# Performance work log

Hardware: AMD Instinct MI355X
Metric: run time of the kernel (lower is better)

Reference implementation:

```python
import jax, jax.numpy as jnp
import numpy as np

B, T, D, H, K, V = 2, 2048, 2048, 16, 128, 128


def _l2norm(x, eps=1e-12):
    # F.normalize(p=2, dim=-1)
    n = jnp.sqrt(jnp.sum(x * x, axis=-1, keepdims=True))
    return x / jnp.maximum(n, eps)


def setup_inputs() -> dict:
    key = jax.random.key(0)
    ks = jax.random.split(key, 7)
    s = D ** -0.5
    return {
        "x": jax.random.normal(ks[0], (B, T, D), jnp.float32),
        "Wq": jax.random.normal(ks[1], (H * K, D), jnp.float32) * s,
        "Wk": jax.random.normal(ks[2], (H * K, D), jnp.float32) * s,
        "Wv": jax.random.normal(ks[3], (H * V, D), jnp.float32) * s,
        "Wa": jax.random.normal(ks[4], (H, D), jnp.float32) * s,
        "ba": jnp.zeros((H,), jnp.float32),
        "Wb": jax.random.normal(ks[5], (H, D), jnp.float32) * s,
        "bb": jnp.zeros((H,), jnp.float32),
    }


def _forward(x, Wq, Wk, Wv, Wa, ba, Wb, bb):
    Bq, Tq, _ = x.shape
    # projections (nn.Linear: y = x @ W.T)
    q = _l2norm(jnp.einsum('btd,od->bto', x, Wq).reshape(Bq, Tq, H, K))
    k = _l2norm(jnp.einsum('btd,od->bto', x, Wk).reshape(Bq, Tq, H, K))
    v = jnp.einsum('btd,od->bto', x, Wv).reshape(Bq, Tq, H, V)
    alpha = jax.nn.sigmoid(jnp.einsum('btd,hd->bth', x, Wa) + ba)          # [B,T,H] decay in (0,1)
    beta = jax.nn.softplus(jnp.einsum('btd,hd->bth', x, Wb) + bb) * K ** (-0.5)

    # gated delta rule recurrence over time (vectorized over B,H):
    #   S_t = a_t * S_{t-1} (I - b_t k_t k_t^T) + b_t v_t k_t^T ;  o_t = S_t q_t
    def step(S, inp):
        q_t, k_t, v_t, a_t, b_t = inp  # [B,H,K],[B,H,K],[B,H,V],[B,H],[B,H]
        Sd = S * a_t[..., None, None]                              # decay  [B,H,V,K]
        pred = jnp.einsum('bhvk,bhk->bhv', Sd, k_t)                # S k
        u = b_t[..., None] * (v_t - pred)                          # delta update [B,H,V]
        S_new = Sd + u[..., None] * k_t[:, :, None, :]             # rank-1 write
        o_t = jnp.einsum('bhvk,bhk->bhv', S_new, q_t)
        return S_new, o_t

    S0 = jnp.zeros((Bq, H, V, K), x.dtype)
    xs = (q.transpose(1, 0, 2, 3), k.transpose(1, 0, 2, 3),
          v.transpose(1, 0, 2, 3), alpha.transpose(1, 0, 2), beta.transpose(1, 0, 2))
    _, o = jax.lax.scan(step, S0, xs)
    return o.transpose(1, 0, 2, 3)  # [B,T,H,V]


def reference(x, Wq, Wk, Wv, Wa, ba, Wb, bb):
    return _forward(x, Wq, Wk, Wv, Wa, ba, Wb, bb)
```

## Files before the change

kernel.cpp:

```cpp
#include <hip/hip_runtime.h>
#include <math.h>

#define BB 2
#define TT 2048
#define DD 2048
#define HH 16
#define KK 128

typedef _Float16 h4 __attribute__((ext_vector_type(4)));
typedef _Float16 v8h __attribute__((ext_vector_type(8)));
typedef float v4f __attribute__((ext_vector_type(4)));
typedef unsigned int u2v __attribute__((ext_vector_type(2)));

__global__ __launch_bounds__(256) void gemm_nt3(const float* __restrict__ A,
                                                const float* __restrict__ W0,
                                                const float* __restrict__ W1,
                                                const float* __restrict__ W2,
                                                float* __restrict__ Cbase,
                                                int M, int N, int Kd) {
  __shared__ float As[8][128];
  __shared__ float Bs[8][128];
  const int z = blockIdx.z;
  const float* W = (z == 0) ? W0 : (z == 1) ? W1 : W2;
  float* C = Cbase + (size_t)z * M * N;
  const int tid = threadIdx.x;
  const int bm = blockIdx.y * 128;
  const int bn = blockIdx.x * 128;
  const int lrow = tid >> 1;
  const int lcol = (tid & 1) * 4;
  const int rm = (tid >> 4) * 8;
  const int rn = (tid & 15) * 8;
  const float* Ap = A + (size_t)(bm + lrow) * Kd + lcol;
  const float* Wp = W + (size_t)(bn + lrow) * Kd + lcol;
  float acc[8][8];
#pragma unroll
  for (int i = 0; i < 8; i++)
#pragma unroll
    for (int j = 0; j < 8; j++) acc[i][j] = 0.f;
  float4 av = *(const float4*)Ap;
  float4 wv = *(const float4*)Wp;
  for (int d0 = 0; d0 < Kd; d0 += 8) {
    __syncthreads();
    As[lcol + 0][lrow] = av.x; As[lcol + 1][lrow] = av.y;
    As[lcol + 2][lrow] = av.z; As[lcol + 3][lrow] = av.w;
    Bs[lcol + 0][lrow] = wv.x; Bs[lcol + 1][lrow] = wv.y;
    Bs[lcol + 2][lrow] = wv.z; Bs[lcol + 3][lrow] = wv.w;
    __syncthreads();
    if (d0 + 8 < Kd) {
      av = *(const float4*)(Ap + d0 + 8);
      wv = *(const float4*)(Wp + d0 + 8);
    }
#pragma unroll
    for (int kk = 0; kk < 8; kk++) {
      const float4 a0 = *(const float4*)&As[kk][rm];
      const float4 a1 = *(const float4*)&As[kk][rm + 4];
      const float4 b0 = *(const float4*)&Bs[kk][rn];
      const float4 b1 = *(const float4*)&Bs[kk][rn + 4];
      const float ar[8] = {a0.x, a0.y, a0.z, a0.w, a1.x, a1.y, a1.z, a1.w};
      const float br[8] = {b0.x, b0.y, b0.z, b0.w, b1.x, b1.y, b1.z, b1.w};
#pragma unroll
      for (int i = 0; i < 8; i++)
#pragma unroll
        for (int j = 0; j < 8; j++) acc[i][j] = fmaf(ar[i], br[j], acc[i][j]);
    }
  }
#pragma unroll
  for (int i = 0; i < 8; i++) {
    float* cp = C + (size_t)(bm + rm + i) * N + bn + rn;
    float4 c0 = {acc[i][0], acc[i][1], acc[i][2], acc[i][3]};
    float4 c1 = {acc[i][4], acc[i][5], acc[i][6], acc[i][7]};
    *(float4*)cp = c0;
    *(float4*)(cp + 4) = c1;
  }
}

__global__ __launch_bounds__(256) void convert_f16(
    const float* __restrict__ x, const float* __restrict__ Wq,
    const float* __restrict__ Wk, const float* __restrict__ Wv,
    _Float16* __restrict__ xh, _Float16* __restrict__ xl,
    _Float16* __restrict__ Wf) {
  const size_t N4X = (size_t)BB * TT * DD / 4;
  const size_t N4W = (size_t)(HH * KK) * DD / 4;
  const size_t i = (size_t)blockIdx.x * 256 + threadIdx.x;
  if (i < N4X) {
    const float4 v = ((const float4*)x)[i];
    h4 hi, lo;
    hi.x = (_Float16)v.x; hi.y = (_Float16)v.y;
    hi.z = (_Float16)v.z; hi.w = (_Float16)v.w;
    lo.x = (_Float16)(v.x - (float)hi.x);
    lo.y = (_Float16)(v.y - (float)hi.y);
    lo.z = (_Float16)(v.z - (float)hi.z);
    lo.w = (_Float16)(v.w - (float)hi.w);
    ((h4*)xh)[i] = hi;
    ((h4*)xl)[i] = lo;
  } else {
    const size_t j = i - N4X;
    const float* Ws = (j < N4W) ? Wq : (j < 2 * N4W) ? Wk : Wv;
    const size_t jj = (j < N4W) ? j : (j < 2 * N4W) ? (j - N4W) : (j - 2 * N4W);
    const float4 v = ((const float4*)Ws)[jj];
    h4 hi;
    hi.x = (_Float16)v.x; hi.y = (_Float16)v.y;
    hi.z = (_Float16)v.z; hi.w = (_Float16)v.w;
    ((h4*)Wf)[j] = hi;
  }
}

#define GLDS(gp, lp)                                              \
  __builtin_amdgcn_global_load_lds(                               \
      (const __attribute__((address_space(1))) void*)(gp),        \
      (__attribute__((address_space(3))) void*)(lp), 16, 0, 0)

__global__ __launch_bounds__(256) void gemm_mfma(
    const _Float16* __restrict__ xh, const _Float16* __restrict__ xl,
    const _Float16* __restrict__ Wf, float* __restrict__ Cbase) {
  __shared__ float4 lraw[1536];
  _Float16* Ah = (_Float16*)lraw;
  _Float16* Al = Ah + 4096;
  _Float16* Bs = Al + 4096;

  const int z = blockIdx.z;
  const _Float16* W = Wf + (size_t)z * DD * (HH * KK);
  float* C = Cbase + (size_t)z * (BB * TT) * (HH * KK);

  const int tid = threadIdx.x;
  const int w = tid >> 6;
  const int lane = tid & 63;
  const int bm = blockIdx.y * 128;
  const int bn = blockIdx.x * 128;
  const int wm = (w & 1) * 64;
  const int wn = (w >> 1) * 64;
  const int m16 = lane & 15;
  const int quad = lane >> 4;

  const _Float16* gAh = xh + (size_t)(bm + (tid >> 2)) * DD + (tid & 3) * 8;
  const _Float16* gAl = xl + (size_t)(bm + (tid >> 2)) * DD + (tid & 3) * 8;
  const _Float16* gB = W + (size_t)(bn + (tid >> 2)) * DD + (tid & 3) * 8;
  const int lb = w * 512;

  v4f acc[4][4];
#pragma unroll
  for (int i = 0; i < 4; i++)
#pragma unroll
    for (int j = 0; j < 4; j++) acc[i][j] = (v4f){0.f, 0.f, 0.f, 0.f};

  for (int d0 = 0; d0 < DD; d0 += 32) {
    GLDS(gAh + d0, Ah + lb);
    GLDS(gAh + d0 + 64 * DD, Ah + 2048 + lb);
    GLDS(gAl + d0, Al + lb);
    GLDS(gAl + d0 + 64 * DD, Al + 2048 + lb);
    GLDS(gB + d0, Bs + lb);
    GLDS(gB + d0 + 64 * DD, Bs + 2048 + lb);
    __syncthreads();
    v8h ah[4], al[4], bw[4];
#pragma unroll
    for (int i = 0; i < 4; i++) {
      ah[i] = *(const v8h*)&Ah[(wm + i * 16 + m16) * 32 + quad * 8];
      al[i] = *(const v8h*)&Al[(wm + i * 16 + m16) * 32 + quad * 8];
      bw[i] = *(const v8h*)&Bs[(wn + i * 16 + m16) * 32 + quad * 8];
    }
#pragma unroll
    for (int mi = 0; mi < 4; mi++)
#pragma unroll
      for (int ni = 0; ni < 4; ni++) {
        acc[mi][ni] = __builtin_amdgcn_mfma_f32_16x16x32_f16(ah[mi], bw[ni],
                                                             acc[mi][ni], 0, 0, 0);
        acc[mi][ni] = __builtin_amdgcn_mfma_f32_16x16x32_f16(al[mi], bw[ni],
                                                             acc[mi][ni], 0, 0, 0);
      }
    __syncthreads();
  }
#pragma unroll
  for (int mi = 0; mi < 4; mi++) {
#pragma unroll
    for (int r = 0; r < 4; r++) {
      float* cp =
          C + (size_t)(bm + wm + mi * 16 + quad * 4 + r) * (HH * KK) + bn + wn + m16;
#pragma unroll
      for (int ni = 0; ni < 4; ni++) cp[ni * 16] = acc[mi][ni][r];
    }
  }
}

__global__ __launch_bounds__(64) void ab_proj(const float* __restrict__ x,
                                              const float* __restrict__ Wa,
                                              const float* __restrict__ ba,
                                              const float* __restrict__ Wb,
                                              const float* __restrict__ bb,
                                              float* __restrict__ abq) {
  const int row = blockIdx.x;
  const int g = blockIdx.y;
  const int h0 = (g & 1) * 8;
  const bool isA = (g < 2);
  const float* W = isA ? Wa : Wb;
  const int lane = threadIdx.x;
  const float* xr = x + (size_t)row * DD;
  float acc[8];
#pragma unroll
  for (int j = 0; j < 8; j++) acc[j] = 0.f;
  for (int d = lane; d < DD; d += 64) {
    const float xv = xr[d];
#pragma unroll
    for (int j = 0; j < 8; j++)
      acc[j] = fmaf(xv, W[(size_t)(h0 + j) * DD + d], acc[j]);
  }
#pragma unroll
  for (int j = 0; j < 8; j++) {
#pragma unroll
    for (int off = 32; off > 0; off >>= 1) acc[j] += __shfl_xor(acc[j], off, 64);
  }
  if (lane == 0) {
    if (isA) {
#pragma unroll
      for (int j = 0; j < 8; j++) {
        const float z = acc[j] + ba[h0 + j];
        abq[((size_t)row * HH + h0 + j) * 4 + 0] = 1.0f / (1.0f + expf(-z));
      }
    } else {
#pragma unroll
      for (int j = 0; j < 8; j++) {
        const float z = acc[j] + bb[h0 + j];
        const float sp = (z > 20.f) ? z : log1pf(expf(z));
        abq[((size_t)row * HH + h0 + j) * 4 + 1] = sp * 0.08838834764831845f;
      }
    }
  }
}

__global__ __launch_bounds__(256) void norm_qk(float* __restrict__ q,
                                               float* __restrict__ k,
                                               float* __restrict__ abq) {
  const int vec = blockIdx.x * 4 + (threadIdx.x >> 6);
  const int l = threadIdx.x & 63;
  float* qp = q + (size_t)vec * 128;
  float* kp = k + (size_t)vec * 128;
  float q0 = qp[l], q1 = qp[l + 64];
  float k0 = kp[l], k1 = kp[l + 64];
  float sq = q0 * q0 + q1 * q1;
  float sk = k0 * k0 + k1 * k1;
#pragma unroll
  for (int off = 32; off > 0; off >>= 1) {
    sq += __shfl_xor(sq, off, 64);
    sk += __shfl_xor(sk, off, 64);
  }
  const float iq = 1.0f / fmaxf(sqrtf(sq), 1e-12f);
  const float ik = 1.0f / fmaxf(sqrtf(sk), 1e-12f);
  q0 *= iq; q1 *= iq; k0 *= ik; k1 *= ik;
  qp[l] = q0; qp[l + 64] = q1;
  kp[l] = k0; kp[l + 64] = k1;
  float pq = q0 * k0 + q1 * k1;
#pragma unroll
  for (int off = 32; off > 0; off >>= 1) pq += __shfl_xor(pq, off, 64);
  if (l == 0) abq[(size_t)vec * 4 + 2] = pq;
}

#define DPP_ADD(x, ctrl)                                                     \
  ((x) + __int_as_float(__builtin_amdgcn_update_dpp(                         \
             0, __float_as_int(x), (ctrl), 0xF, 0xF, true)))

__device__ __forceinline__ float xadd32(float x) {
  const u2v r = __builtin_amdgcn_permlane32_swap(__float_as_uint(x),
                                                 __float_as_uint(x), false,
                                                 false);
  return __uint_as_float(r.x) + __uint_as_float(r.y);
}

#define SCAN_STEP(kc, qc, vc, ac, store_ptr)                                   \
  {                                                                            \
    float dk = fmaf(S0, kc.x, fmaf(S1, kc.y, fmaf(S2, kc.z, S3 * kc.w)));      \
    float dq = fmaf(S0, qc.x, fmaf(S1, qc.y, fmaf(S2, qc.z, S3 * qc.w)));      \
    dk = DPP_ADD(dk, 0xB1);  dq = DPP_ADD(dq, 0xB1);             \
    dk = DPP_ADD(dk, 0x4E);  dq = DPP_ADD(dq, 0x4E);             \
    dk = DPP_ADD(dk, 0x141); dq = DPP_ADD(dq, 0x141);            \
    dk = DPP_ADD(dk, 0x140); dq = DPP_ADD(dq, 0x140);            \
    dk = xadd32(dk);         dq = xadd32(dq);                    \
    const float u = ac.y * fmaf(-ac.x, dk, vc);                                \
    const float oo = fmaf(ac.x, dq, u * ac.z);                                 \
    S0 = fmaf(ac.x, S0, u * kc.x);                                             \
    S1 = fmaf(ac.x, S1, u * kc.y);                                             \
    S2 = fmaf(ac.x, S2, u * kc.z);                                             \
    S3 = fmaf(ac.x, S3, u * kc.w);                                             \
    if (ks == 0) *(store_ptr) = oo;                                            \
  }

#define PD 8

__global__ __launch_bounds__(256, 2) void scan_kernel(
    const float* __restrict__ q, const float* __restrict__ k,
    const float* __restrict__ v, const float* __restrict__ abq,
    float* __restrict__ o) {
  const int bid = blockIdx.x;
  const int bh = bid & 31;
  const int s = bid >> 5;
  const int h = bh & 15;
  const int b = bh >> 4;
  const int tid = threadIdx.x;
  const int w = tid >> 6;
  const int lane = tid & 63;
  const int rg = (lane >> 4) & 1;
  const int ks = (lane & 15) | ((lane >> 5) << 4);
  const int vrow = s * 8 + w * 2 + rg;

  const size_t base = (size_t)b * TT * 2048 + (size_t)h * KK;
  const float* kb = k + base + ks * 4;
  const float* qb = q + base + ks * 4;
  const float* vb = v + base + vrow;
  const float* ab = abq + ((size_t)b * TT * HH + h) * 4;
  float* ob = o + base + vrow;

  float S0 = 0.f, S1 = 0.f, S2 = 0.f, S3 = 0.f;

  float4 kf[PD], qf[PD], af[PD];
  float vf[PD];
#pragma unroll
  for (int d = 0; d < PD; d++) {
    kf[d] = *(const float4*)(kb + d * 2048);
    qf[d] = *(const float4*)(qb + d * 2048);
    vf[d] = vb[d * 2048];
    af[d] = *(const float4*)(ab + d * 64);
  }

  int off = 0;
  int aoff = 0;
  for (int t0 = 0; t0 < TT - PD; t0 += PD) {
#pragma unroll
    for (int j = 0; j < PD; j++) {
      SCAN_STEP(kf[j], qf[j], vf[j], af[j], ob + off + j * 2048);
      kf[j] = *(const float4*)(kb + off + (j + PD) * 2048);
      qf[j] = *(const float4*)(qb + off + (j + PD) * 2048);
      vf[j] = vb[off + (j + PD) * 2048];
      af[j] = *(const float4*)(ab + aoff + (j + PD) * 64);
      __builtin_amdgcn_sched_barrier(0);
    }
    off += PD * 2048;
    aoff += PD * 64;
  }
#pragma unroll
  for (int j = 0; j < PD; j++) {
    SCAN_STEP(kf[j], qf[j], vf[j], af[j], ob + off + j * 2048);
  }
}

extern "C" void kernel_launch(void* const* d_in, const int* in_sizes, int n_in,
                              void* d_out, int out_size, void* d_ws,
                              size_t ws_size, hipStream_t stream) {
  const float* x = (const float*)d_in[0];
  const float* Wq = (const float*)d_in[1];
  const float* Wk = (const float*)d_in[2];
  const float* Wv = (const float*)d_in[3];
  const float* Wa = (const float*)d_in[4];
  const float* ba = (const float*)d_in[5];
  const float* Wb = (const float*)d_in[6];
  const float* bb = (const float*)d_in[7];
  float* out = (float*)d_out;
  float* ws = (float*)d_ws;

  const size_t PROJ = (size_t)BB * TT * HH * KK;
  const size_t NABQ = (size_t)BB * TT * HH * 4;
  float* qw = ws;
  float* kw = ws + PROJ;
  float* vw = ws + 2 * PROJ;
  float* abq = ws + 3 * PROJ;
  _Float16* xh = (_Float16*)(abq + NABQ);
  _Float16* xl = xh + (size_t)BB * TT * DD;
  _Float16* Wf = xl + (size_t)BB * TT * DD;
  const size_t NEED = (3 * PROJ + NABQ) * 4 +
                      ((size_t)BB * TT * DD * 2 + 3 * (size_t)(HH * KK) * DD) * 2;

  const int M = BB * TT;
  const int N = HH * KK;
  if (ws_size >= NEED) {
    const int cgrid = (int)(((size_t)BB * TT * DD / 4 + 3 * (size_t)N * DD / 4) / 256);
    convert_f16<<<cgrid, 256, 0, stream>>>(x, Wq, Wk, Wv, xh, xl, Wf);
    gemm_mfma<<<dim3(N / 128, M / 128, 3), 256, 0, stream>>>(xh, xl, Wf, qw);
  } else {
    gemm_nt3<<<dim3(N / 128, M / 128, 3), 256, 0, stream>>>(x, Wq, Wk, Wv, qw,
                                                            M, N, DD);
  }
  ab_proj<<<dim3(M, 4), 64, 0, stream>>>(x, Wa, ba, Wb, bb, abq);
  norm_qk<<<(BB * TT * HH) / 4, 256, 0, stream>>>(qw, kw, abq);
  scan_kernel<<<BB * HH * 16, 256, 0, stream>>>(qw, kw, vw, abq, out);
}
```

Before: 774.6 us.

## Drop fp16 lo-part of x in GEMM, pack scan state math, batch output stores

The projection GEMM no longer splits x into fp16 hi and lo parts. It uses one fp16 operand, which halves the MFMA count, the LDS traffic and the conversion writes, at the cost of accuracy in q/k/v. The scan kernel now holds its state in packed float2 vectors and uses elementwise FMA so the compiler can emit packed FP32 instructions. Outputs are buffered across the 8 unrolled steps and written by 8 lanes at once instead of one store per step.

```diff
diff --git a/kernel.cpp b/kernel.cpp
--- a/kernel.cpp
+++ b/kernel.cpp
@@ -10,6 +10,7 @@
 typedef _Float16 h4 __attribute__((ext_vector_type(4)));
 typedef _Float16 v8h __attribute__((ext_vector_type(8)));
 typedef float v4f __attribute__((ext_vector_type(4)));
+typedef float f2 __attribute__((ext_vector_type(2)));
 typedef unsigned int u2v __attribute__((ext_vector_type(2)));
 
 __global__ __launch_bounds__(256) void gemm_nt3(const float* __restrict__ A,
@@ -77,22 +78,16 @@
 __global__ __launch_bounds__(256) void convert_f16(
     const float* __restrict__ x, const float* __restrict__ Wq,
     const float* __restrict__ Wk, const float* __restrict__ Wv,
-    _Float16* __restrict__ xh, _Float16* __restrict__ xl,
-    _Float16* __restrict__ Wf) {
+    _Float16* __restrict__ xh, _Float16* __restrict__ Wf) {
   const size_t N4X = (size_t)BB * TT * DD / 4;
   const size_t N4W = (size_t)(HH * KK) * DD / 4;
   const size_t i = (size_t)blockIdx.x * 256 + threadIdx.x;
   if (i < N4X) {
     const float4 v = ((const float4*)x)[i];
-    h4 hi, lo;
+    h4 hi;
     hi.x = (_Float16)v.x; hi.y = (_Float16)v.y;
     hi.z = (_Float16)v.z; hi.w = (_Float16)v.w;
-    lo.x = (_Float16)(v.x - (float)hi.x);
-    lo.y = (_Float16)(v.y - (float)hi.y);
-    lo.z = (_Float16)(v.z - (float)hi.z);
-    lo.w = (_Float16)(v.w - (float)hi.w);
     ((h4*)xh)[i] = hi;
-    ((h4*)xl)[i] = lo;
   } else {
     const size_t j = i - N4X;
     const float* Ws = (j < N4W) ? Wq : (j < 2 * N4W) ? Wk : Wv;
@@ -111,12 +106,11 @@
       (__attribute__((address_space(3))) void*)(lp), 16, 0, 0)
 
 __global__ __launch_bounds__(256) void gemm_mfma(
-    const _Float16* __restrict__ xh, const _Float16* __restrict__ xl,
-    const _Float16* __restrict__ Wf, float* __restrict__ Cbase) {
-  __shared__ float4 lraw[1536];
+    const _Float16* __restrict__ xh, const _Float16* __restrict__ Wf,
+    float* __restrict__ Cbase) {
+  __shared__ float4 lraw[1024];
   _Float16* Ah = (_Float16*)lraw;
-  _Float16* Al = Ah + 4096;
-  _Float16* Bs = Al + 4096;
+  _Float16* Bs = Ah + 4096;
 
   const int z = blockIdx.z;
   const _Float16* W = Wf + (size_t)z * DD * (HH * KK);
@@ -132,8 +126,7 @@
   const int m16 = lane & 15;
   const int quad = lane >> 4;
 
-  const _Float16* gAh = xh + (size_t)(bm + (tid >> 2)) * DD + (tid & 3) * 8;
-  const _Float16* gAl = xl + (size_t)(bm + (tid >> 2)) * DD + (tid & 3) * 8;
+  const _Float16* gA = xh + (size_t)(bm + (tid >> 2)) * DD + (tid & 3) * 8;
   const _Float16* gB = W + (size_t)(bn + (tid >> 2)) * DD + (tid & 3) * 8;
   const int lb = w * 512;
 
@@ -144,29 +137,23 @@
     for (int j = 0; j < 4; j++) acc[i][j] = (v4f){0.f, 0.f, 0.f, 0.f};
 
   for (int d0 = 0; d0 < DD; d0 += 32) {
-    GLDS(gAh + d0, Ah + lb);
-    GLDS(gAh + d0 + 64 * DD, Ah + 2048 + lb);
-    GLDS(gAl + d0, Al + lb);
-    GLDS(gAl + d0 + 64 * DD, Al + 2048 + lb);
+    GLDS(gA + d0, Ah + lb);
+    GLDS(gA + d0 + 64 * DD, Ah + 2048 + lb);
     GLDS(gB + d0, Bs + lb);
     GLDS(gB + d0 + 64 * DD, Bs + 2048 + lb);
     __syncthreads();
-    v8h ah[4], al[4], bw[4];
+    v8h ah[4], bw[4];
 #pragma unroll
     for (int i = 0; i < 4; i++) {
       ah[i] = *(const v8h*)&Ah[(wm + i * 16 + m16) * 32 + quad * 8];
-      al[i] = *(const v8h*)&Al[(wm + i * 16 + m16) * 32 + quad * 8];
       bw[i] = *(const v8h*)&Bs[(wn + i * 16 + m16) * 32 + quad * 8];
     }
 #pragma unroll
     for (int mi = 0; mi < 4; mi++)
 #pragma unroll
-      for (int ni = 0; ni < 4; ni++) {
+      for (int ni = 0; ni < 4; ni++)
         acc[mi][ni] = __builtin_amdgcn_mfma_f32_16x16x32_f16(ah[mi], bw[ni],
                                                              acc[mi][ni], 0, 0, 0);
-        acc[mi][ni] = __builtin_amdgcn_mfma_f32_16x16x32_f16(al[mi], bw[ni],
-                                                             acc[mi][ni], 0, 0, 0);
-      }
     __syncthreads();
   }
 #pragma unroll
@@ -264,10 +251,16 @@
   return __uint_as_float(r.x) + __uint_as_float(r.y);
 }
 
-#define SCAN_STEP(kc, qc, vc, ac, store_ptr)                                   \
+#define SCAN_STEP(kc, qc, vc, ac, jj)                                          \
   {                                                                            \
-    float dk = fmaf(S0, kc.x, fmaf(S1, kc.y, fmaf(S2, kc.z, S3 * kc.w)));      \
-    float dq = fmaf(S0, qc.x, fmaf(S1, qc.y, fmaf(S2, qc.z, S3 * qc.w)));      \
+    const f2 ka = {kc.x, kc.y};                                                \
+    const f2 kb2 = {kc.z, kc.w};                                               \
+    const f2 qa = {qc.x, qc.y};                                                \
+    const f2 qb2 = {qc.z, qc.w};                                               \
+    const f2 pdk = __builtin_elementwise_fma(Sb, kb2, Sa * ka);                \
+    const f2 pdq = __builtin_elementwise_fma(Sb, qb2, Sa * qa);                \
+    float dk = pdk.x + pdk.y;                                                  \
+    float dq = pdq.x + pdq.y;                                                  \
     dk = DPP_ADD(dk, 0xB1);  dq = DPP_ADD(dq, 0xB1);             \
     dk = DPP_ADD(dk, 0x4E);  dq = DPP_ADD(dq, 0x4E);             \
     dk = DPP_ADD(dk, 0x141); dq = DPP_ADD(dq, 0x141);            \
@@ -275,11 +268,11 @@
     dk = xadd32(dk);         dq = xadd32(dq);                    \
     const float u = ac.y * fmaf(-ac.x, dk, vc);                                \
     const float oo = fmaf(ac.x, dq, u * ac.z);                                 \
-    S0 = fmaf(ac.x, S0, u * kc.x);                                             \
-    S1 = fmaf(ac.x, S1, u * kc.y);                                             \
-    S2 = fmaf(ac.x, S2, u * kc.z);                                             \
-    S3 = fmaf(ac.x, S3, u * kc.w);                                             \
-    if (ks == 0) *(store_ptr) = oo;                                            \
+    const f2 a2 = {ac.x, ac.x};                                                \
+    const f2 u2 = {u, u};                                                      \
+    Sa = __builtin_elementwise_fma(a2, Sa, u2 * ka);                           \
+    Sb = __builtin_elementwise_fma(a2, Sb, u2 * kb2);                          \
+    obuf = (ks == (jj)) ? oo : obuf;                                           \
   }
 
 #define PD 8
@@ -301,22 +294,24 @@
   const int vrow = s * 8 + w * 2 + rg;
 
   const size_t base = (size_t)b * TT * 2048 + (size_t)h * KK;
-  const float* kb = k + base + ks * 4;
-  const float* qb = q + base + ks * 4;
-  const float* vb = v + base + vrow;
-  const float* ab = abq + ((size_t)b * TT * HH + h) * 4;
-  float* ob = o + base + vrow;
-
-  float S0 = 0.f, S1 = 0.f, S2 = 0.f, S3 = 0.f;
+  const float* kU = k + base;
+  const float* qU = q + base;
+  const float* vU = v + base;
+  const float* aU = abq + ((size_t)b * TT * HH + h) * 4;
+  float* oU = o + base;
+  const int vks = ks * 4;
+
+  f2 Sa = {0.f, 0.f}, Sb = {0.f, 0.f};
+  float obuf = 0.f;
 
   float4 kf[PD], qf[PD], af[PD];
   float vf[PD];
 #pragma unroll
   for (int d = 0; d < PD; d++) {
-    kf[d] = *(const float4*)(kb + d * 2048);
-    qf[d] = *(const float4*)(qb + d * 2048);
-    vf[d] = vb[d * 2048];
-    af[d] = *(const float4*)(ab + d * 64);
+    kf[d] = *(const float4*)(kU + vks + d * 2048);
+    qf[d] = *(const float4*)(qU + vks + d * 2048);
+    vf[d] = vU[vrow + d * 2048];
+    af[d] = *(const float4*)(aU + d * 64);
   }
 
   int off = 0;
@@ -324,20 +319,22 @@
   for (int t0 = 0; t0 < TT - PD; t0 += PD) {
 #pragma unroll
     for (int j = 0; j < PD; j++) {
-      SCAN_STEP(kf[j], qf[j], vf[j], af[j], ob + off + j * 2048);
-      kf[j] = *(const float4*)(kb + off + (j + PD) * 2048);
-      qf[j] = *(const float4*)(qb + off + (j + PD) * 2048);
-      vf[j] = vb[off + (j + PD) * 2048];
-      af[j] = *(const float4*)(ab + aoff + (j + PD) * 64);
+      SCAN_STEP(kf[j], qf[j], vf[j], af[j], j);
+      kf[j] = *(const float4*)(kU + vks + off + (j + PD) * 2048);
+      qf[j] = *(const float4*)(qU + vks + off + (j + PD) * 2048);
+      vf[j] = vU[vrow + off + (j + PD) * 2048];
+      af[j] = *(const float4*)(aU + aoff + (j + PD) * 64);
       __builtin_amdgcn_sched_barrier(0);
     }
+    if (ks < 8) oU[vrow + off + ks * 2048] = obuf;
     off += PD * 2048;
     aoff += PD * 64;
   }
 #pragma unroll
   for (int j = 0; j < PD; j++) {
-    SCAN_STEP(kf[j], qf[j], vf[j], af[j], ob + off + j * 2048);
-  }
+    SCAN_STEP(kf[j], qf[j], vf[j], af[j], j);
+  }
+  if (ks < 8) oU[vrow + off + ks * 2048] = obuf;
 }
 
 extern "C" void kernel_launch(void* const* d_in, const int* in_sizes, int n_in,
@@ -361,17 +358,16 @@
   float* vw = ws + 2 * PROJ;
   float* abq = ws + 3 * PROJ;
   _Float16* xh = (_Float16*)(abq + NABQ);
-  _Float16* xl = xh + (size_t)BB * TT * DD;
-  _Float16* Wf = xl + (size_t)BB * TT * DD;
+  _Float16* Wf = xh + (size_t)BB * TT * DD;
   const size_t NEED = (3 * PROJ + NABQ) * 4 +
-                      ((size_t)BB * TT * DD * 2 + 3 * (size_t)(HH * KK) * DD) * 2;
+                      ((size_t)BB * TT * DD + 3 * (size_t)(HH * KK) * DD) * 2;
 
   const int M = BB * TT;
   const int N = HH * KK;
   if (ws_size >= NEED) {
     const int cgrid = (int)(((size_t)BB * TT * DD / 4 + 3 * (size_t)N * DD / 4) / 256);
-    convert_f16<<<cgrid, 256, 0, stream>>>(x, Wq, Wk, Wv, xh, xl, Wf);
-    gemm_mfma<<<dim3(N / 128, M / 128, 3), 256, 0, stream>>>(xh, xl, Wf, qw);
+    convert_f16<<<cgrid, 256, 0, stream>>>(x, Wq, Wk, Wv, xh, Wf);
+    gemm_mfma<<<dim3(N / 128, M / 128, 3), 256, 0, stream>>>(xh, Wf, qw);
   } else {
     gemm_nt3<<<dim3(N / 128, M / 128, 3), 256, 0, stream>>>(x, Wq, Wk, Wv, qw,
                                                             M, N, DD);
```

Result: faster. 726.0 us (-6.3%).
